# Performance work log

Measured on AMD Instinct MI355X. Metric: run time of the kernel, lower is better.

## Reference

```python
import jax, jax.numpy as jnp
import numpy as np

# static config matching init_kwargs
NODE, K, KER, STR = 32, 10, 5, 2
B, C = 8, 64
N = NODE * NODE          # 1024 nodes per sample
BN = B * N               # 8192 total nodes
OUT = (NODE - KER) // STR + 1
E = OUT * OUT            # local hyperedges per sample (196)
BN_EPS = 1e-5


def _local_block_diag():
    """Static block-diagonal local incidence matrix (BN, B*E), built once in numpy."""
    idx = np.arange(N).reshape(NODE, NODE)
    H_local = np.zeros((N, E), np.float32)
    e = 0
    for i in range(0, NODE - KER + 1, STR):
        for j in range(0, NODE - KER + 1, STR):
            H_local[idx[i:i + KER, j:j + KER].ravel(), e] = 1.0
            e += 1
    blk = np.zeros((BN, B * E), np.float32)
    for b in range(B):
        blk[b * N:(b + 1) * N, b * E:(b + 1) * E] = H_local
    return jnp.asarray(blk)


_LOCAL_BLK = _local_block_diag()


def setup_inputs() -> dict:
    key = jax.random.key(0)
    k1, k2 = jax.random.split(key, 2)
    x = jax.random.normal(k1, (B, N, C), jnp.float32)
    W_conv = jax.random.normal(k2, (C, C), jnp.float32) * 0.05
    b_conv = jnp.zeros((C,), jnp.float32)
    gamma = jnp.ones((C,), jnp.float32)
    beta = jnp.zeros((C,), jnp.float32)
    return {"x": x, "W_conv": W_conv, "b_conv": b_conv, "gamma": gamma, "beta": beta}


def reference(x, W_conv, b_conv, gamma, beta):
    xm = x.reshape(BN, C)                       # merged nodes (B*N, C)

    # --- hypergraph construction (no_grad in torch) ---
    xs = jax.lax.stop_gradient(xm)
    sq = jnp.sum(xs * xs, axis=-1, keepdims=True)
    dists = sq - 2.0 * (xs @ xs.T) + sq.T       # (BN, BN) pairwise sq-dists
    _, inds = jax.lax.top_k(-dists, K + 1)      # K+1 smallest distances
    # weights_function(prob=False) -> all ones; scatter incidence
    H = jnp.zeros((BN, BN), x.dtype).at[jnp.arange(BN)[:, None], inds].set(1.0)
    # Dv == K+1 for every row -> max_k = K+1 and the second topk gives new_H == H
    Hfull = jnp.concatenate([H, _LOCAL_BLK], axis=1)  # (BN, BN + B*E)

    # G = Dv^{-1/2} H W De^{-1} H^T Dv^{-1/2}, W = I, via diagonal scaling
    DV = Hfull.sum(axis=1)
    DE = jnp.maximum(Hfull.sum(axis=0), 1e-8)
    dv2 = DV ** -0.5
    A = dv2[:, None] * Hfull
    G = (A * (1.0 / DE)[None, :]) @ A.T          # (BN, BN)
    G = jax.lax.stop_gradient(G)

    # --- HGNN conv: linear -> G matmul -> BN (train stats) -> relu -> residual ---
    y = xm @ W_conv.T + b_conv                   # (BN, C)
    z = G @ y                                    # (BN, C)
    mu = z.mean(axis=0)
    var = z.var(axis=0)                          # biased, as torch BN training
    zn = (z - mu) / jnp.sqrt(var + BN_EPS) * gamma + beta
    out = jax.nn.relu(zn) + xm
    return out.reshape(B, N, C)
```

## Files before the change

### kernel.cpp

```cpp
#include <hip/hip_runtime.h>
#include <math.h>

#define BNTOT 8192
#define CH    64
#define KP1   11
#define NLOC  1568
#define MARGIN 1.0f
#define LCAPR 1024

typedef __attribute__((ext_vector_type(8))) short short8;
typedef __attribute__((ext_vector_type(4))) float float4v;

__device__ __forceinline__ int pcnt(int p) {
  int lo = p - 4; if (lo < 0) lo = 0; lo += (lo & 1);
  int hi = p; if (hi > 26) hi = 26;
  return (hi >= lo) ? (((hi - lo) >> 1) + 1) : 0;
}
__device__ __forceinline__ float dv2_of(int u) {
  int node = u & 1023;
  int rr = node >> 5, cc = node & 31;
  int dv = KP1 + pcnt(rr) * pcnt(cc);
  return 1.0f / sqrtf((float)dv);
}
__device__ __forceinline__ unsigned short f2bf(float f) {
  unsigned u = __float_as_uint(f);
  unsigned r = (u + 0x7FFFu + ((u >> 16) & 1u)) >> 16;
  return (unsigned short)r;
}
__device__ __forceinline__ unsigned long long skey(float s, int idx) {
  unsigned u = __float_as_uint(s);
  u = (u & 0x80000000u) ? ~u : (u | 0x80000000u);
  return ((unsigned long long)u << 32) | (unsigned)idx;
}

__global__ void k_cast(const float* __restrict__ X, unsigned short* __restrict__ Xh,
                       float* __restrict__ sq) {
  int g = blockIdx.x * 256 + threadIdx.x;
  int lane = threadIdx.x & 63;
  float v = X[g];
  Xh[g] = f2bf(v);
  float s = v * v;
  #pragma unroll
  for (int off = 32; off >= 1; off >>= 1) s += __shfl_xor(s, off, 64);
  if (lane == 0) sq[g >> 6] = s;
}

__global__ __launch_bounds__(256)
void k_thrpart(const float* __restrict__ X, const float* __restrict__ sq,
               float* __restrict__ part) {
  const int tid = threadIdx.x, wave = tid >> 6, lane = tid & 63;
  const int rg = blockIdx.x >> 3, chunk = blockIdx.x & 7;
  const int row = rg * 64 + lane;
  float xr[CH];
  {
    const float4* xp = (const float4*)(X + (size_t)row * CH);
    #pragma unroll
    for (int k = 0; k < CH / 4; ++k) {
      float4 v = xp[k];
      xr[4*k+0] = v.x; xr[4*k+1] = v.y; xr[4*k+2] = v.z; xr[4*k+3] = v.w;
    }
  }
  float tv[KP1];
  #pragma unroll
  for (int t = 0; t < KP1; ++t) tv[t] = INFINITY;

  for (int s = 0; s < 32; ++s) {
    int j = __builtin_amdgcn_readfirstlane(((chunk * 4 + wave) * 32 + s) * 8);
    const float* cp = X + (size_t)j * CH;
    float d0 = 0.f, d1 = 0.f, d2 = 0.f, d3 = 0.f;
    #pragma unroll
    for (int k = 0; k < CH / 4; ++k) {
      d0 = fmaf(xr[4*k+0], cp[4*k+0], d0);
      d1 = fmaf(xr[4*k+1], cp[4*k+1], d1);
      d2 = fmaf(xr[4*k+2], cp[4*k+2], d2);
      d3 = fmaf(xr[4*k+3], cp[4*k+3], d3);
    }
    float cv = fmaf(-2.0f, (d0 + d1) + (d2 + d3), sq[j]);
    #pragma unroll
    for (int t = 0; t < KP1; ++t) {
      float lo = fminf(tv[t], cv), hi = fmaxf(tv[t], cv);
      tv[t] = lo; cv = hi;
    }
  }
  __shared__ float ls[4][64][KP1];
  #pragma unroll
  for (int t = 0; t < KP1; ++t) ls[wave][lane][t] = tv[t];
  __syncthreads();
  if (tid < 64) {
    float v[KP1];
    #pragma unroll
    for (int t = 0; t < KP1; ++t) v[t] = ls[0][tid][t];
    #pragma unroll
    for (int w = 1; w < 4; ++w)
      #pragma unroll
      for (int t = 0; t < KP1; ++t) {
        float cv = ls[w][tid][t];
        #pragma unroll
        for (int s2 = 0; s2 < KP1; ++s2) {
          float lo = fminf(v[s2], cv), hi = fmaxf(v[s2], cv);
          v[s2] = lo; cv = hi;
        }
      }
    size_t base = ((size_t)blockIdx.x * 64 + tid) * KP1;
    #pragma unroll
    for (int t = 0; t < KP1; ++t) part[base + t] = v[t];
  }
}

__global__ void k_thrmerge(const float* __restrict__ part, float* __restrict__ thr) {
  const int rg = blockIdx.x, lane = threadIdx.x;
  const int row = rg * 64 + lane;
  float v[KP1];
  {
    size_t b0 = ((size_t)(rg * 8) * 64 + lane) * KP1;
    #pragma unroll
    for (int t = 0; t < KP1; ++t) v[t] = part[b0 + t];
  }
  for (int c = 1; c < 8; ++c) {
    size_t b = ((size_t)(rg * 8 + c) * 64 + lane) * KP1;
    #pragma unroll
    for (int t = 0; t < KP1; ++t) {
      float cv = part[b + t];
      #pragma unroll
      for (int s2 = 0; s2 < KP1; ++s2) {
        float lo = fminf(v[s2], cv), hi = fmaxf(v[s2], cv);
        v[s2] = lo; cv = hi;
      }
    }
  }
  thr[row] = v[KP1 - 1] + MARGIN;
}

__global__ __launch_bounds__(256)
void k_filter(const unsigned short* __restrict__ Xh, const float* __restrict__ sq,
              const float* __restrict__ thr, unsigned long long* __restrict__ mask) {
  const int tid = threadIdx.x, wave = tid >> 6, lane = tid & 63;
  const int m = lane & 15, q = lane >> 4;
  const int rowbase = (blockIdx.x >> 5) * 64;
  const int colbase = (blockIdx.x & 31) * 256 + wave * 64;
  const int wcol = (blockIdx.x & 31) * 4 + wave;

  short8 a[4][2];
  #pragma unroll
  for (int rt = 0; rt < 4; ++rt)
    #pragma unroll
    for (int kc = 0; kc < 2; ++kc)
      a[rt][kc] = *(const short8*)(Xh + (size_t)(rowbase + rt * 16 + m) * CH + kc * 32 + q * 8);

  short8 b0[4], b1[4];
  float sqv[4];
  #pragma unroll
  for (int sub = 0; sub < 4; ++sub) {
    const int coln = colbase + sub * 16 + m;
    const short8* bp = (const short8*)(Xh + (size_t)coln * CH + q * 8);
    b0[sub] = bp[0];
    b1[sub] = bp[4];
    sqv[sub] = sq[coln];
  }

  float thrv[16];
  #pragma unroll
  for (int rt = 0; rt < 4; ++rt)
    #pragma unroll
    for (int r = 0; r < 4; ++r)
      thrv[rt * 4 + r] = thr[rowbase + rt * 16 + q * 4 + r];

  const float4v cz = {0.f, 0.f, 0.f, 0.f};
  const int sr = lane & 15, qq = sr >> 2, rr = sr & 3;

  #pragma unroll
  for (int rt = 0; rt < 4; ++rt) {
    unsigned long long bal[4][4];
    #pragma unroll
    for (int sub = 0; sub < 4; ++sub) {
      float4v c = __builtin_amdgcn_mfma_f32_16x16x32_bf16(a[rt][0], b0[sub], cz, 0, 0, 0);
      c = __builtin_amdgcn_mfma_f32_16x16x32_bf16(a[rt][1], b1[sub], c, 0, 0, 0);
      #pragma unroll
      for (int r = 0; r < 4; ++r) {
        float score = fmaf(-2.0f, c[r], sqv[sub]);
        bal[sub][r] = __ballot(score < thrv[rt * 4 + r]);
      }
    }
    unsigned long long w = 0;
    #pragma unroll
    for (int sub = 0; sub < 4; ++sub) {
      unsigned long long bsel = (rr == 0) ? bal[sub][0]
                              : (rr == 1) ? bal[sub][1]
                              : (rr == 2) ? bal[sub][2]
                              :             bal[sub][3];
      unsigned long long slice = (bsel >> (qq * 16)) & 0xFFFFull;
      w |= slice << (sub * 16);
    }
    if ((lane >> 4) == rt)
      mask[(size_t)(rowbase + rt * 16 + sr) * 128 + wcol] = w;
  }
}

__global__ __launch_bounds__(256)
void k_rescore(const float* __restrict__ X, const float* __restrict__ sq,
               const unsigned long long* __restrict__ mask,
               int* __restrict__ inds, int* __restrict__ DE) {
  __shared__ int cols[4][LCAPR];
  const int tid = threadIdx.x, lane = tid & 63, wv = tid >> 6;
  const int row = __builtin_amdgcn_readfirstlane(blockIdx.x * 4 + wv);

  float xr[CH];
  {
    const float4* xp = (const float4*)(X + (size_t)row * CH);
    #pragma unroll
    for (int k = 0; k < CH / 4; ++k) {
      float4 v = xp[k];
      xr[4*k+0] = v.x; xr[4*k+1] = v.y; xr[4*k+2] = v.z; xr[4*k+3] = v.w;
    }
  }

  const unsigned long long* mrow = mask + (size_t)row * 128;
  unsigned long long w0 = mrow[lane * 2 + 0];
  unsigned long long w1 = mrow[lane * 2 + 1];

  int cnt = __popcll(w0) + __popcll(w1);
  int pfx = cnt;
  #pragma unroll
  for (int off = 1; off < 64; off <<= 1) {
    int o = __shfl_up(pfx, off, 64);
    pfx += (lane >= off) ? o : 0;
  }
  const int total = __shfl(pfx, 63, 64);
  int p = pfx - cnt;

  if (total <= LCAPR) {
    unsigned long long w = w0;
    while (w) { int b = __builtin_ctzll(w); w &= w - 1; cols[wv][p++] = lane * 128 + b; }
    w = w1;
    while (w) { int b = __builtin_ctzll(w); w &= w - 1; cols[wv][p++] = lane * 128 + 64 + b; }
  }
  __syncthreads();

  float tv[KP1]; int ti[KP1];
  #pragma unroll
  for (int t = 0; t < KP1; ++t) { tv[t] = INFINITY; ti[t] = -1; }

  if (total <= LCAPR) {
    for (int s = lane; s < total; s += 64) {
      int cj = cols[wv][s];
      const float4* cp = (const float4*)(X + (size_t)cj * CH);
      float d0 = 0.f, d1 = 0.f, d2 = 0.f, d3 = 0.f;
      #pragma unroll
      for (int k = 0; k < CH / 4; ++k) {
        float4 v = cp[k];
        d0 = fmaf(xr[4*k+0], v.x, d0);
        d1 = fmaf(xr[4*k+1], v.y, d1);
        d2 = fmaf(xr[4*k+2], v.z, d2);
        d3 = fmaf(xr[4*k+3], v.w, d3);
      }
      float score = fmaf(-2.0f, (d0 + d1) + (d2 + d3), sq[cj]);
      if (score < tv[KP1 - 1]) {
        float cv = score; int ci = cj;
        #pragma unroll
        for (int t = 0; t < KP1; ++t) {
          bool sw = cv < tv[t];
          float nv = sw ? cv    : tv[t]; int ni = sw ? ci    : ti[t];
          float ov = sw ? tv[t] : cv;    int oi = sw ? ti[t] : ci;
          tv[t] = nv; ti[t] = ni; cv = ov; ci = oi;
        }
      }
    }
  } else {
    for (int s = lane; s < BNTOT; s += 64) {
      const float4* cp = (const float4*)(X + (size_t)s * CH);
      float d0 = 0.f, d1 = 0.f, d2 = 0.f, d3 = 0.f;
      #pragma unroll
      for (int k = 0; k < CH / 4; ++k) {
        float4 v = cp[k];
        d0 = fmaf(xr[4*k+0], v.x, d0);
        d1 = fmaf(xr[4*k+1], v.y, d1);
        d2 = fmaf(xr[4*k+2], v.z, d2);
        d3 = fmaf(xr[4*k+3], v.w, d3);
      }
      float score = fmaf(-2.0f, (d0 + d1) + (d2 + d3), sq[s]);
      if (score < tv[KP1 - 1]) {
        float cv = score; int ci = s;
        #pragma unroll
        for (int t = 0; t < KP1; ++t) {
          bool sw = cv < tv[t];
          float nv = sw ? cv    : tv[t]; int ni = sw ? ci    : ti[t];
          float ov = sw ? tv[t] : cv;    int oi = sw ? ti[t] : ci;
          tv[t] = nv; ti[t] = ni; cv = ov; ci = oi;
        }
      }
    }
  }

  unsigned long long cur = skey(tv[0], ti[0]);
  unsigned long long keep = 0;
  #pragma unroll
  for (int t = 0; t < KP1; ++t) {
    unsigned long long mw = cur;
    #pragma unroll
    for (int off = 1; off < 64; off <<= 1) {
      unsigned lo = __shfl_xor((unsigned)mw, off, 64);
      unsigned hi = __shfl_xor((unsigned)(mw >> 32), off, 64);
      unsigned long long o = ((unsigned long long)hi << 32) | lo;
      mw = (o < mw) ? o : mw;
    }
    if (lane == t) keep = mw;
    if (cur == mw) {
      #pragma unroll
      for (int q = 0; q < KP1 - 1; ++q) { tv[q] = tv[q+1]; ti[q] = ti[q+1]; }
      tv[KP1-1] = INFINITY; ti[KP1-1] = -1;
      cur = skey(tv[0], ti[0]);
    }
  }
  if (lane < KP1) {
    int idx = (int)(unsigned)(keep & 0xFFFFFFFFull);
    inds[(size_t)row * KP1 + lane] = idx;
    atomicAdd(&DE[idx], 1);
  }
}

__global__ void k_lin(const float* __restrict__ X, const float* __restrict__ W,
                      const float* __restrict__ bias, float* __restrict__ t) {
  int lane = threadIdx.x & 63;
  int wave = threadIdx.x >> 6;
  int rowbase = (blockIdx.x * 4 + wave) * 4;
  float wr[CH];
  {
    const float4* wp = (const float4*)(W + (size_t)lane * CH);
    #pragma unroll
    for (int k = 0; k < CH / 4; ++k) {
      float4 v = wp[k];
      wr[4*k+0] = v.x; wr[4*k+1] = v.y; wr[4*k+2] = v.z; wr[4*k+3] = v.w;
    }
  }
  float bc = bias[lane];
  #pragma unroll
  for (int r = 0; r < 4; ++r) {
    int row = __builtin_amdgcn_readfirstlane(rowbase + r);
    const float* xp = X + (size_t)row * CH;
    float d0 = 0.f, d1 = 0.f, d2 = 0.f, d3 = 0.f;
    #pragma unroll
    for (int k = 0; k < CH / 4; ++k) {
      d0 = fmaf(wr[4*k+0], xp[4*k+0], d0);
      d1 = fmaf(wr[4*k+1], xp[4*k+1], d1);
      d2 = fmaf(wr[4*k+2], xp[4*k+2], d2);
      d3 = fmaf(wr[4*k+3], xp[4*k+3], d3);
    }
    float y = (d0 + d1) + (d2 + d3) + bc;
    t[(size_t)row * CH + lane] = y * dv2_of(row);
  }
}

__global__ void k_edge(const float* __restrict__ t, const int* __restrict__ inds,
                       float* __restrict__ s_knn, float* __restrict__ s_loc) {
  int c = threadIdx.x & 63;
  int w = threadIdx.x >> 6;
  if (blockIdx.x < BNTOT / 4) {
    int u = blockIdx.x * 4 + w;
    float val = t[(size_t)u * CH + c];
    int ub = __builtin_amdgcn_readfirstlane(u);
    const int* ip = inds + (size_t)ub * KP1;
    #pragma unroll
    for (int j = 0; j < KP1; ++j) {
      int e = ip[j];
      atomicAdd(&s_knn[(size_t)e * CH + c], val);
    }
  } else {
    int e = (blockIdx.x - BNTOT / 4) * 4 + w;
    int b  = e / 196;
    int le = e - b * 196;
    int pi = le / 14;
    int pj = le - pi * 14;
    int base = b * 1024 + (pi * 2) * 32 + pj * 2;
    float acc = 0.f;
    #pragma unroll
    for (int di = 0; di < 5; ++di)
      #pragma unroll
      for (int dj = 0; dj < 5; ++dj)
        acc += t[(size_t)(base + di * 32 + dj) * CH + c];
    s_loc[(size_t)e * CH + c] = acc * (1.0f / 25.0f);
  }
}

__global__ void k_gatherbn(const float* __restrict__ s_knn, const float* __restrict__ s_loc,
                           const int* __restrict__ inds, const int* __restrict__ DE,
                           float* __restrict__ z, float* __restrict__ part,
                           float* __restrict__ partsq) {
  int c = threadIdx.x & 63;
  int w = threadIdx.x >> 6;
  int u = blockIdx.x * 4 + w;
  int ub = __builtin_amdgcn_readfirstlane(u);
  const int* ip = inds + (size_t)ub * KP1;
  float acc = 0.f;
  #pragma unroll
  for (int j = 0; j < KP1; ++j) {
    int e = ip[j];
    float invde = 1.0f / (float)DE[e];
    acc += s_knn[(size_t)e * CH + c] * invde;
  }
  int node = ub & 1023, b = ub >> 10;
  int rr = node >> 5, cc = node & 31;
  int i0 = rr - 4; if (i0 < 0) i0 = 0; i0 += (i0 & 1);
  int i1 = rr; if (i1 > 26) i1 = 26;
  int j0 = cc - 4; if (j0 < 0) j0 = 0; j0 += (j0 & 1);
  int j1 = cc; if (j1 > 26) j1 = 26;
  for (int i = i0; i <= i1; i += 2)
    for (int jj = j0; jj <= j1; jj += 2) {
      int e = b * 196 + (i >> 1) * 14 + (jj >> 1);
      acc += s_loc[(size_t)e * CH + c];
    }
  float zv = acc * dv2_of(ub);
  z[(size_t)ub * CH + c] = zv;

  __shared__ float ls[4][CH], ls2[4][CH];
  ls[w][c] = zv; ls2[w][c] = zv * zv;
  __syncthreads();
  if (threadIdx.x < 64) {
    part[(size_t)blockIdx.x * CH + c]   = ls[0][c] + ls[1][c] + ls[2][c] + ls[3][c];
    partsq[(size_t)blockIdx.x * CH + c] = ls2[0][c] + ls2[1][c] + ls2[2][c] + ls2[3][c];
  }
}

__global__ void k_bnfin1(const float* __restrict__ part, const float* __restrict__ partsq,
                         float* __restrict__ part2, float* __restrict__ partsq2) {
  int c = threadIdx.x & 63;
  int rq = threadIdx.x >> 6;
  int blk = blockIdx.x;
  float s = 0.f, s2 = 0.f;
  for (int k = 0; k < 16; ++k) {
    size_t r = (size_t)(blk * 64 + rq * 16 + k) * CH + c;
    s += part[r]; s2 += partsq[r];
  }
  __shared__ float ls[4][CH], ls2[4][CH];
  ls[rq][c] = s; ls2[rq][c] = s2;
  __syncthreads();
  if (rq == 0) {
    part2[(size_t)blk * CH + c]   = ls[0][c] + ls[1][c] + ls[2][c] + ls[3][c];
    partsq2[(size_t)blk * CH + c] = ls2[0][c] + ls2[1][c] + ls2[2][c] + ls2[3][c];
  }
}

__global__ void k_out(const float* __restrict__ z, const float* __restrict__ X,
                      const float* __restrict__ part2, const float* __restrict__ partsq2,
                      const float* __restrict__ gamma, const float* __restrict__ beta,
                      float* __restrict__ out) {
  __shared__ float ls[4][CH], ls2[4][CH], smu[CH], srstd[CH];
  int c = threadIdx.x & 63;
  int w = threadIdx.x >> 6;
  float s = 0.f, s2 = 0.f;
  #pragma unroll
  for (int b = 0; b < 8; ++b) {
    size_t r = (size_t)(w * 8 + b) * CH + c;
    s += part2[r]; s2 += partsq2[r];
  }
  ls[w][c] = s; ls2[w][c] = s2;
  __syncthreads();
  if (threadIdx.x < 64) {
    float S  = ls[0][c] + ls[1][c] + ls[2][c] + ls[3][c];
    float S2 = ls2[0][c] + ls2[1][c] + ls2[2][c] + ls2[3][c];
    float m = S * (1.0f / (float)BNTOT);
    float var = S2 * (1.0f / (float)BNTOT) - m * m;
    smu[c] = m;
    srstd[c] = 1.0f / sqrtf(var + 1e-5f);
  }
  __syncthreads();

  int u = blockIdx.x * 4 + w;
  size_t idx = (size_t)u * CH + c;
  float zn = (z[idx] - smu[c]) * srstd[c] * gamma[c] + beta[c];
  out[idx] = fmaxf(zn, 0.f) + X[idx];
}

extern "C" void kernel_launch(void* const* d_in, const int* in_sizes, int n_in,
                              void* d_out, int out_size, void* d_ws, size_t ws_size,
                              hipStream_t stream) {
  const float* X     = (const float*)d_in[0];
  const float* W     = (const float*)d_in[1];
  const float* bias  = (const float*)d_in[2];
  const float* gamma = (const float*)d_in[3];
  const float* beta  = (const float*)d_in[4];
  float* out = (float*)d_out;

  float* ws = (float*)d_ws;
  float* sq      = ws;
  float* thr     = sq + 8192;
  float* t       = thr + 8192;
  float* s_loc   = t + 524288;
  float* z       = s_loc + 100352;
  float* part    = z + 524288;
  float* partsq  = part + 131072;
  float* part2   = partsq + 131072;
  float* partsq2 = part2 + 2048;
  float* thrpart = partsq2 + 2048;
  int*   inds    = (int*)(thrpart + 720896);
  unsigned short* Xh = (unsigned short*)(inds + 90112);
  unsigned long long* mask = (unsigned long long*)(Xh + 524288);
  int*   DE     = (int*)(mask + (size_t)8192 * 128);
  float* s_knn  = (float*)(DE + 8192);

  hipMemsetAsync(DE, 0, (size_t)(8192 + 524288) * 4, stream);

  k_cast    <<<2048, 256, 0, stream>>>(X, Xh, sq);
  k_thrpart <<<1024, 256, 0, stream>>>(X, sq, thrpart);
  k_thrmerge<<<128, 64, 0, stream>>>(thrpart, thr);
  k_filter  <<<4096, 256, 0, stream>>>(Xh, sq, thr, mask);
  k_rescore <<<2048, 256, 0, stream>>>(X, sq, mask, inds, DE);
  k_lin     <<<512, 256, 0, stream>>>(X, W, bias, t);
  k_edge    <<<BNTOT / 4 + NLOC / 4, 256, 0, stream>>>(t, inds, s_knn, s_loc);
  k_gatherbn<<<BNTOT / 4, 256, 0, stream>>>(s_knn, s_loc, inds, DE, z, part, partsq);
  k_bnfin1  <<<32, 256, 0, stream>>>(part, partsq, part2, partsq2);
  k_out     <<<BNTOT / 4, 256, 0, stream>>>(z, X, part2, partsq2, gamma, beta, out);

  (void)in_sizes; (void)n_in; (void)out_size; (void)ws_size;
}
```

Measured before the change: 232.2 us.

## Replace per-lane top-K insertion with wave-wide radix threshold selection in candidate refine

The exact-distance refine kernel now computes a prefix sum with bit-sliced ballots and mbcnt instead of a shuffle scan. For the candidate path it stores up to four scores per lane as orderable keys, then finds the K+1 threshold with a 32-step ballot binary search over key values and an index tie-break search, and writes the winners via ballot compaction. This avoids the per-lane sorted insertion and the 11-round shuffle merge. The candidate cap drops from 1024 to 256, so rows with more candidates fall back to the full brute-force scan, which risks more slow-path rows.

```diff
diff --git a/kernel.cpp b/kernel.cpp
--- a/kernel.cpp
+++ b/kernel.cpp
@@ -6,7 +6,7 @@
 #define KP1   11
 #define NLOC  1568
 #define MARGIN 1.0f
-#define LCAPR 1024
+#define LCAPR 256
 
 typedef __attribute__((ext_vector_type(8))) short short8;
 typedef __attribute__((ext_vector_type(4))) float float4v;
@@ -27,10 +27,16 @@
   unsigned r = (u + 0x7FFFu + ((u >> 16) & 1u)) >> 16;
   return (unsigned short)r;
 }
+__device__ __forceinline__ unsigned fkey(float s) {
+  unsigned u = __float_as_uint(s);
+  return (u & 0x80000000u) ? ~u : (u | 0x80000000u);
+}
 __device__ __forceinline__ unsigned long long skey(float s, int idx) {
-  unsigned u = __float_as_uint(s);
-  u = (u & 0x80000000u) ? ~u : (u | 0x80000000u);
-  return ((unsigned long long)u << 32) | (unsigned)idx;
+  return ((unsigned long long)fkey(s) << 32) | (unsigned)idx;
+}
+__device__ __forceinline__ int mbcnt64(unsigned long long m) {
+  return __builtin_amdgcn_mbcnt_hi((unsigned)(m >> 32),
+         __builtin_amdgcn_mbcnt_lo((unsigned)m, 0));
 }
 
 __global__ void k_cast(const float* __restrict__ X, unsigned short* __restrict__ Xh,
@@ -219,53 +225,94 @@
   unsigned long long w1 = mrow[lane * 2 + 1];
 
   int cnt = __popcll(w0) + __popcll(w1);
-  int pfx = cnt;
-  #pragma unroll
-  for (int off = 1; off < 64; off <<= 1) {
-    int o = __shfl_up(pfx, off, 64);
-    pfx += (lane >= off) ? o : 0;
-  }
-  const int total = __shfl(pfx, 63, 64);
-  int p = pfx - cnt;
+  int p = 0, total = 0;
+  #pragma unroll
+  for (int b = 0; b < 8; ++b) {
+    unsigned long long bb = __ballot((cnt >> b) & 1);
+    p     += mbcnt64(bb) << b;
+    total += __popcll(bb) << b;
+  }
 
   if (total <= LCAPR) {
     unsigned long long w = w0;
     while (w) { int b = __builtin_ctzll(w); w &= w - 1; cols[wv][p++] = lane * 128 + b; }
     w = w1;
     while (w) { int b = __builtin_ctzll(w); w &= w - 1; cols[wv][p++] = lane * 128 + 64 + b; }
-  }
-  __syncthreads();
-
-  float tv[KP1]; int ti[KP1];
-  #pragma unroll
-  for (int t = 0; t < KP1; ++t) { tv[t] = INFINITY; ti[t] = -1; }
-
-  if (total <= LCAPR) {
-    for (int s = lane; s < total; s += 64) {
-      int cj = cols[wv][s];
-      const float4* cp = (const float4*)(X + (size_t)cj * CH);
-      float d0 = 0.f, d1 = 0.f, d2 = 0.f, d3 = 0.f;
-      #pragma unroll
-      for (int k = 0; k < CH / 4; ++k) {
-        float4 v = cp[k];
-        d0 = fmaf(xr[4*k+0], v.x, d0);
-        d1 = fmaf(xr[4*k+1], v.y, d1);
-        d2 = fmaf(xr[4*k+2], v.z, d2);
-        d3 = fmaf(xr[4*k+3], v.w, d3);
-      }
-      float score = fmaf(-2.0f, (d0 + d1) + (d2 + d3), sq[cj]);
-      if (score < tv[KP1 - 1]) {
-        float cv = score; int ci = cj;
+
+    unsigned kscore[4]; int kidx[4];
+    #pragma unroll
+    for (int a = 0; a < 4; ++a) { kscore[a] = 0xFFFFFFFFu; kidx[a] = 0; }
+    const int slots = (total + 63) >> 6;
+    for (int a = 0; a < slots; ++a) {
+      int s = a * 64 + lane;
+      if (s < total) {
+        int cj = cols[wv][s];
+        const float4* cp = (const float4*)(X + (size_t)cj * CH);
+        float d0 = 0.f, d1 = 0.f, d2 = 0.f, d3 = 0.f;
         #pragma unroll
-        for (int t = 0; t < KP1; ++t) {
-          bool sw = cv < tv[t];
-          float nv = sw ? cv    : tv[t]; int ni = sw ? ci    : ti[t];
-          float ov = sw ? tv[t] : cv;    int oi = sw ? ti[t] : ci;
-          tv[t] = nv; ti[t] = ni; cv = ov; ci = oi;
+        for (int k = 0; k < CH / 4; ++k) {
+          float4 v = cp[k];
+          d0 = fmaf(xr[4*k+0], v.x, d0);
+          d1 = fmaf(xr[4*k+1], v.y, d1);
+          d2 = fmaf(xr[4*k+2], v.z, d2);
+          d3 = fmaf(xr[4*k+3], v.w, d3);
         }
-      }
+        float score = fmaf(-2.0f, (d0 + d1) + (d2 + d3), sq[cj]);
+        kscore[a] = fkey(score);
+        kidx[a] = cj;
+      }
+    }
+
+    unsigned long long blo = 0, bhi = 1ull << 32;
+    #pragma unroll 4
+    for (int it = 0; it < 32; ++it) {
+      unsigned mid = (unsigned)((blo + bhi) >> 1);
+      int l = (kscore[0] < mid) + (kscore[1] < mid) + (kscore[2] < mid) + (kscore[3] < mid);
+      int c = __popcll(__ballot(l & 1)) + 2 * __popcll(__ballot(l & 2))
+            + 4 * __popcll(__ballot(l & 4));
+      if (c < KP1) blo = mid; else bhi = mid;
+    }
+    const unsigned T = (unsigned)blo;
+
+    int ll = (kscore[0] < T) + (kscore[1] < T) + (kscore[2] < T) + (kscore[3] < T);
+    int c_less = __popcll(__ballot(ll & 1)) + 2 * __popcll(__ballot(ll & 2))
+               + 4 * __popcll(__ballot(ll & 4));
+    int le = (kscore[0] <= T) + (kscore[1] <= T) + (kscore[2] <= T) + (kscore[3] <= T);
+    int c_le = __popcll(__ballot(le & 1)) + 2 * __popcll(__ballot(le & 2))
+             + 4 * __popcll(__ballot(le & 4));
+    const int needed = KP1 - c_less;
+    const int cnt_eq = c_le - c_less;
+
+    unsigned idxcut = BNTOT;
+    if (cnt_eq != needed) {
+      int lo2 = 0, hi2 = BNTOT;
+      for (int it = 0; it < 13; ++it) {
+        int mid2 = (lo2 + hi2) >> 1;
+        int l2 = ((kscore[0] == T) & (kidx[0] < mid2)) + ((kscore[1] == T) & (kidx[1] < mid2))
+               + ((kscore[2] == T) & (kidx[2] < mid2)) + ((kscore[3] == T) & (kidx[3] < mid2));
+        int c2 = __popcll(__ballot(l2 & 1)) + 2 * __popcll(__ballot(l2 & 2))
+               + 4 * __popcll(__ballot(l2 & 4));
+        if (c2 < needed) lo2 = mid2; else hi2 = mid2;
+      }
+      idxcut = (unsigned)hi2;
+    }
+
+    int base = 0;
+    #pragma unroll
+    for (int a = 0; a < 4; ++a) {
+      bool win = (kscore[a] < T) | ((kscore[a] == T) & ((unsigned)kidx[a] < idxcut));
+      unsigned long long bal = __ballot(win);
+      int pos = base + mbcnt64(bal);
+      if (win) {
+        inds[(size_t)row * KP1 + pos] = kidx[a];
+        atomicAdd(&DE[kidx[a]], 1);
+      }
+      base += __popcll(bal);
     }
   } else {
+    float tv[KP1]; int ti[KP1];
+    #pragma unroll
+    for (int t = 0; t < KP1; ++t) { tv[t] = INFINITY; ti[t] = -1; }
     for (int s = lane; s < BNTOT; s += 64) {
       const float4* cp = (const float4*)(X + (size_t)s * CH);
       float d0 = 0.f, d1 = 0.f, d2 = 0.f, d3 = 0.f;
@@ -283,38 +330,38 @@
         #pragma unroll
         for (int t = 0; t < KP1; ++t) {
           bool sw = cv < tv[t];
-          float nv = sw ? cv    : tv[t]; int ni = sw ? ci    : ti[t];
+          float nv = sw ? cv    : tv[t]; int ni = sw ? ti[t] : ti[t];
+          ni = sw ? ci : ti[t];
           float ov = sw ? tv[t] : cv;    int oi = sw ? ti[t] : ci;
           tv[t] = nv; ti[t] = ni; cv = ov; ci = oi;
         }
       }
     }
-  }
-
-  unsigned long long cur = skey(tv[0], ti[0]);
-  unsigned long long keep = 0;
-  #pragma unroll
-  for (int t = 0; t < KP1; ++t) {
-    unsigned long long mw = cur;
-    #pragma unroll
-    for (int off = 1; off < 64; off <<= 1) {
-      unsigned lo = __shfl_xor((unsigned)mw, off, 64);
-      unsigned hi = __shfl_xor((unsigned)(mw >> 32), off, 64);
-      unsigned long long o = ((unsigned long long)hi << 32) | lo;
-      mw = (o < mw) ? o : mw;
-    }
-    if (lane == t) keep = mw;
-    if (cur == mw) {
+    unsigned long long cur = skey(tv[0], ti[0]);
+    unsigned long long keep = 0;
+    #pragma unroll
+    for (int t = 0; t < KP1; ++t) {
+      unsigned long long mw = cur;
       #pragma unroll
-      for (int q = 0; q < KP1 - 1; ++q) { tv[q] = tv[q+1]; ti[q] = ti[q+1]; }
-      tv[KP1-1] = INFINITY; ti[KP1-1] = -1;
-      cur = skey(tv[0], ti[0]);
-    }
-  }
-  if (lane < KP1) {
-    int idx = (int)(unsigned)(keep & 0xFFFFFFFFull);
-    inds[(size_t)row * KP1 + lane] = idx;
-    atomicAdd(&DE[idx], 1);
+      for (int off = 1; off < 64; off <<= 1) {
+        unsigned lo = __shfl_xor((unsigned)mw, off, 64);
+        unsigned hi = __shfl_xor((unsigned)(mw >> 32), off, 64);
+        unsigned long long o = ((unsigned long long)hi << 32) | lo;
+        mw = (o < mw) ? o : mw;
+      }
+      if (lane == t) keep = mw;
+      if (cur == mw) {
+        #pragma unroll
+        for (int q = 0; q < KP1 - 1; ++q) { tv[q] = tv[q+1]; ti[q] = ti[q+1]; }
+        tv[KP1-1] = INFINITY; ti[KP1-1] = -1;
+        cur = skey(tv[0], ti[0]);
+      }
+    }
+    if (lane < KP1) {
+      int idx = (int)(unsigned)(keep & 0xFFFFFFFFull);
+      inds[(size_t)row * KP1 + lane] = idx;
+      atomicAdd(&DE[idx], 1);
+    }
   }
 }
 
```

Result: no change. 232.9 us (+0.3%).
